# Performance work log

Measured on AMD Instinct MI355X. Metric: run time of the kernel, lower is better.

The kernel has to match this reference:

```python
import jax, jax.numpy as jnp
import numpy as np

HEADS = 16
KV_HEADS = 4
DIM_HEAD = 64
DIM = 1024
B, N = 2, 2048


def setup_inputs() -> dict:
    key = jax.random.key(0)
    k1, k2, k3 = jax.random.split(key, 3)
    x = jax.random.normal(k1, (B, N, DIM), dtype=jnp.float32)
    Wq = jax.random.normal(k2, (DIM, HEADS * DIM_HEAD), dtype=jnp.float32) / np.sqrt(DIM)
    Wkv = jax.random.normal(k3, (DIM, 2 * KV_HEADS * DIM_HEAD), dtype=jnp.float32) / np.sqrt(DIM)
    k_scale = jnp.ones((HEADS, 1, DIM_HEAD), dtype=jnp.float32)
    return {"x": x, "Wq": Wq, "Wkv": Wkv, "k_scale": k_scale}


def reference(x, Wq, Wkv, k_scale):
    b, n, _ = x.shape
    g = HEADS // KV_HEADS  # query heads per kv head
    scale = DIM_HEAD ** -0.5
    # fused qkv projections (no bias)
    q = (x @ Wq).reshape(b, n, HEADS, DIM_HEAD)
    kv = x @ Wkv
    k, v = jnp.split(kv, 2, axis=-1)
    k = k.reshape(b, n, KV_HEADS, DIM_HEAD).transpose(0, 2, 1, 3)  # b k n d
    v = v.reshape(b, n, KV_HEADS, DIM_HEAD).transpose(0, 2, 1, 3)  # b k n d
    # group query heads: b, kv_heads, g, n, d
    qg = q.transpose(0, 2, 1, 3).reshape(b, KV_HEADS, g, n, DIM_HEAD)
    # per-query-head k scale, applied to the group-broadcast k (qk-norm)
    ks = k_scale.reshape(KV_HEADS, g, 1, DIM_HEAD)
    kk = k[:, :, None, :, :] * ks  # b k g n d
    dots = jnp.einsum('bkgid,bkgjd->bkgij', qg, kk) * scale
    attn = jax.nn.softmax(dots, axis=-1)
    out = jnp.einsum('bkgij,bkjd->bkgid', attn, v)  # v broadcast over g
    out = out.reshape(b, HEADS, n, DIM_HEAD).transpose(0, 2, 1, 3).reshape(b, n, HEADS * DIM_HEAD)
    return out
```

## Files before the change

### kernel.cpp

```cpp
#include <hip/hip_runtime.h>
#include <stdint.h>
#include <math.h>

typedef __attribute__((ext_vector_type(8))) __bf16 bf16x8;
typedef __attribute__((ext_vector_type(4))) float f32x4;
typedef __attribute__((ext_vector_type(16))) float f32x16;

__device__ __forceinline__ uint32_t f32_to_bf16_rne(float f) {
  union { float f; uint32_t u; } v; v.f = f;
  return (v.u + 0x7FFFu + ((v.u >> 16) & 1u)) >> 16;
}

__device__ __forceinline__ uint32_t cvt_pk_bf16(float lo, float hi) {
  uint32_t r;
  asm("v_cvt_pk_bf16_f32 %0, %1, %2" : "=v"(r) : "v"(lo), "v"(hi));
  return r;
}

__device__ __forceinline__ void gld16(void* lds, const void* g) {
  __builtin_amdgcn_global_load_lds(
      (__attribute__((address_space(1))) void*)(g),
      (__attribute__((address_space(3))) void*)(lds), 16, 0, 0);
}

__device__ __forceinline__ f32x4 mfma16(bf16x8 a, bf16x8 b, f32x4 c) {
  return __builtin_amdgcn_mfma_f32_16x16x32_bf16(a, b, c, 0, 0, 0);
}
__device__ __forceinline__ f32x16 mfma32(bf16x8 a, bf16x8 b, f32x16 c) {
  return __builtin_amdgcn_mfma_f32_32x32x16_bf16(a, b, c, 0, 0, 0);
}

#define LOG2E 1.44269504088896340736f

__global__ __launch_bounds__(256) void k_convert_x(const float* __restrict__ x,
                                                   uint16_t* __restrict__ xb) {
  int i = blockIdx.x * 256 + threadIdx.x;
  const float4* xv = (const float4*)x;
  float4 a = xv[2 * i], b2 = xv[2 * i + 1];
  uint32_t w0 = f32_to_bf16_rne(a.x) | (f32_to_bf16_rne(a.y) << 16);
  uint32_t w1 = f32_to_bf16_rne(a.z) | (f32_to_bf16_rne(a.w) << 16);
  uint32_t w2 = f32_to_bf16_rne(b2.x) | (f32_to_bf16_rne(b2.y) << 16);
  uint32_t w3 = f32_to_bf16_rne(b2.z) | (f32_to_bf16_rne(b2.w) << 16);
  ((uint4*)xb)[i] = make_uint4(w0, w1, w2, w3);
}

__global__ __launch_bounds__(256) void k_convert_w(const float* __restrict__ wq,
                                                   const float* __restrict__ wkv,
                                                   uint16_t* __restrict__ wt) {
  __shared__ float tile[64][65];
  int c0 = blockIdx.x * 64, k0 = blockIdx.y * 64;
  int t = threadIdx.x;
  int col = t & 63, rq = t >> 6;
#pragma unroll
  for (int rr = 0; rr < 16; rr++) {
    int r = rr * 4 + rq;
    int c = c0 + col;
    float v = (c < 1024) ? wq[(uint64_t)(k0 + r) * 1024 + c]
                         : wkv[(uint64_t)(k0 + r) * 512 + (c - 1024)];
    tile[r][col] = v;
  }
  __syncthreads();
#pragma unroll
  for (int rr = 0; rr < 16; rr++) {
    int a = rr * 4 + rq;
    wt[(uint64_t)(c0 + a) * 1024 + k0 + col] = (uint16_t)f32_to_bf16_rne(tile[col][a]);
  }
}

__global__ __launch_bounds__(256, 3) void k_proj_gemm(
    const uint16_t* __restrict__ xb, const uint16_t* __restrict__ wt,
    const float* __restrict__ kscale, uint16_t* __restrict__ q_ws,
    uint16_t* __restrict__ kf_ws, uint16_t* __restrict__ vf_ws) {
  __shared__ __align__(16) uint16_t As[2][128 * 32];
  __shared__ __align__(16) uint16_t Bs[2][64 * 32];
  int t = threadIdx.x;
  int w = t >> 6, l = t & 63;
  int lq = l & 15, lg = l >> 4;
  int m0 = blockIdx.x * 128, n0 = blockIdx.y * 64;
  int wr = w >> 1, wc = w & 1;
  f32x4 acc[4][2] = {};

  auto stage = [&](int buf, int k0) {
#pragma unroll
    for (int j = 0; j < 2; j++) {
      int tt = j * 256 + t;
      int r = tt >> 2, s = tt & 3;
      int sl = s ^ ((r >> 1) & 3);
      gld16((char*)&As[buf][0] + (j * 256 + w * 64) * 16,
            xb + (uint64_t)(m0 + r) * 1024 + k0 + sl * 8);
    }
    {
      int r = t >> 2, s = t & 3;
      int sl = s ^ ((r >> 1) & 3);
      gld16((char*)&Bs[buf][0] + (w * 64) * 16,
            wt + (uint64_t)(n0 + r) * 1024 + k0 + sl * 8);
    }
  };

  stage(0, 0);
  asm volatile("s_waitcnt vmcnt(0)" ::: "memory");
  __builtin_amdgcn_s_barrier();
  int cur = 0;
  for (int k0 = 0; k0 < 1024; k0 += 32) {
    if (k0 + 32 < 1024) stage(cur ^ 1, k0 + 32);
    bf16x8 af[4], bfr[2];
#pragma unroll
    for (int m = 0; m < 4; m++) {
      int r = wr * 64 + m * 16 + lq;
      int s = lg ^ ((r >> 1) & 3);
      af[m] = *(const bf16x8*)(&As[cur][r * 32 + s * 8]);
    }
#pragma unroll
    for (int n = 0; n < 2; n++) {
      int r = wc * 32 + n * 16 + lq;
      int s = lg ^ ((r >> 1) & 3);
      bfr[n] = *(const bf16x8*)(&Bs[cur][r * 32 + s * 8]);
    }
    __builtin_amdgcn_s_setprio(1);
#pragma unroll
    for (int m = 0; m < 4; m++)
#pragma unroll
      for (int n = 0; n < 2; n++)
        acc[m][n] = mfma16(af[m], bfr[n], acc[m][n]);
    __builtin_amdgcn_s_setprio(0);
    asm volatile("s_waitcnt vmcnt(0) lgkmcnt(0)" ::: "memory");
    __builtin_amdgcn_s_barrier();
    cur ^= 1;
  }

#pragma unroll
  for (int m = 0; m < 4; m++)
#pragma unroll
    for (int n = 0; n < 2; n++)
#pragma unroll
      for (int jj = 0; jj < 4; jj++) {
        int row = m0 + wr * 64 + m * 16 + 4 * lg + jj;
        int col = n0 + wc * 32 + n * 16 + lq;
        float val = acc[m][n][jj];
        int b = row >> 11, nn = row & 2047;
        if (col < 1024) {
          val *= kscale[col] * 0.125f * LOG2E;
          q_ws[((uint64_t)((b * 16 + (col >> 6)) * 2048 + nn)) * 64 + (col & 63)] =
              (uint16_t)f32_to_bf16_rne(val);
        } else if (col < 1280) {
          int kvh = (col - 1024) >> 6;
          int d = col & 63;
          int gsu = nn >> 5, lrr = nn & 31;
          int mm = d >> 4, hh = (d >> 3) & 1, el = d & 7;
          kf_ws[(uint64_t)(b * 4 + kvh) * 131072 +
                (uint64_t)((((gsu * 4 + mm) * 64) + hh * 32 + lrr) * 8 + el)] =
              (uint16_t)f32_to_bf16_rne(val);
        } else {
          int kvh = (col - 1280) >> 6;
          int d = col & 63;
          int gsu = nn >> 5, jj2 = (nn >> 4) & 1, hh = (nn >> 3) & 1, el = nn & 7;
          int dd = d >> 5, lrr = d & 31;
          vf_ws[(uint64_t)(b * 4 + kvh) * 131072 +
                (uint64_t)((((gsu * 4 + dd * 2 + jj2) * 64) + hh * 32 + lrr) * 8 + el)] =
              (uint16_t)f32_to_bf16_rne(val);
        }
      }
}

__global__ __launch_bounds__(512, 4) void k_attn(const uint16_t* __restrict__ q_ws,
                                                 const uint16_t* __restrict__ kf_ws,
                                                 const uint16_t* __restrict__ vf_ws,
                                                 float* __restrict__ out) {
  __shared__ __align__(16) char smem[33280];

  int t = threadIdx.x, w = t >> 6, l = t & 63;
  int lr = l & 31, hi = l >> 5;
  int wq = w & 3, half = w >> 2;
  int blk = blockIdx.x;
  int c = blk & 7, j = blk >> 3;
  int b = c >> 2, kvh = c & 3;
  int h = kvh * 4 + (j >> 4), qb = j & 15;

  const uint16_t* Qb = q_ws + (uint64_t)(b * 16 + h) * 2048 * 64;
  const uint16_t* Kp =
      kf_ws + (uint64_t)(b * 4 + kvh) * 131072 + (uint64_t)half * 65536 + l * 8;
  const uint16_t* Vp =
      vf_ws + (uint64_t)(b * 4 + kvh) * 131072 + (uint64_t)half * 65536 + l * 8;
  int qrow0 = qb * 128 + wq * 32;

  bf16x8 qfrag[4];
#pragma unroll
  for (int m = 0; m < 4; m++)
    qfrag[m] = *(const bf16x8*)(Qb + (uint64_t)(qrow0 + lr) * 64 + m * 16 + hi * 8);

  f32x16 oacc[2] = {};
  float l_run = 0.f;

  bf16x8 kf[4], vf[4];
#pragma unroll
  for (int i = 0; i < 4; i++) kf[i] = *(const bf16x8*)(Kp + i * 512);
#pragma unroll
  for (int i = 0; i < 4; i++) vf[i] = *(const bf16x8*)(Vp + i * 512);

  for (int su = 0; su < 32; ++su) {
    f32x16 Tacc = {};
    __builtin_amdgcn_s_setprio(1);
#pragma unroll
    for (int m = 0; m < 4; m++) Tacc = mfma32(kf[m], qfrag[m], Tacc);
    __builtin_amdgcn_s_setprio(0);

    if (su != 31) {
#pragma unroll
      for (int i = 0; i < 4; i++)
        kf[i] = *(const bf16x8*)(Kp + (su + 1) * 2048 + i * 512);
    }

    float p[16];
#pragma unroll
    for (int e = 0; e < 16; e++) p[e] = __builtin_amdgcn_exp2f(Tacc[e]);
    float sm0 = ((p[0] + p[1]) + (p[2] + p[3])) + ((p[4] + p[5]) + (p[6] + p[7]));
    float sm1 = ((p[8] + p[9]) + (p[10] + p[11])) + ((p[12] + p[13]) + (p[14] + p[15]));
    l_run += sm0 + sm1;

    bf16x8 pa[2];
#pragma unroll
    for (int jj = 0; jj < 2; jj++) {
      int base = 8 * jj;
      uint32_t wlo0 = cvt_pk_bf16(p[base + 0], p[base + 1]);
      uint32_t wlo1 = cvt_pk_bf16(p[base + 2], p[base + 3]);
      uint32_t whi0 = cvt_pk_bf16(p[base + 4], p[base + 5]);
      uint32_t whi1 = cvt_pk_bf16(p[base + 6], p[base + 7]);
      uint32_t send0 = hi ? wlo0 : whi0;
      uint32_t send1 = hi ? wlo1 : whi1;
      uint32_t recv0 = (uint32_t)__shfl_xor((int)send0, 32);
      uint32_t recv1 = (uint32_t)__shfl_xor((int)send1, 32);
      union { uint32_t u[4]; bf16x8 v; } pu;
      pu.u[0] = hi ? recv0 : wlo0;
      pu.u[1] = hi ? recv1 : wlo1;
      pu.u[2] = hi ? whi0 : recv0;
      pu.u[3] = hi ? whi1 : recv1;
      pa[jj] = pu.v;
    }

    __builtin_amdgcn_s_setprio(1);
#pragma unroll
    for (int dd = 0; dd < 2; dd++)
#pragma unroll
      for (int jj = 0; jj < 2; jj++)
        oacc[dd] = mfma32(pa[jj], vf[dd * 2 + jj], oacc[dd]);
    __builtin_amdgcn_s_setprio(0);

    if (su != 31) {
#pragma unroll
      for (int i = 0; i < 4; i++)
        vf[i] = *(const bf16x8*)(Vp + (su + 1) * 2048 + i * 512);
    }
  }

  l_run += __shfl_xor(l_run, 32);

  float* exch = (float*)smem;
  float* exl = (float*)(smem + 32768);
  if (half == 1) {
#pragma unroll
    for (int r = 0; r < 16; r++) {
      int qr = (r & 3) + 8 * (r >> 2) + 4 * hi;
      exch[wq * 2048 + qr * 64 + lr] = oacc[0][r];
      exch[wq * 2048 + qr * 64 + 32 + lr] = oacc[1][r];
    }
    if (hi == 0) exl[wq * 32 + lr] = l_run;
  }
  __syncthreads();
  if (half == 0) {
    l_run += exl[wq * 32 + lr];
    float inv = 1.0f / l_run;
#pragma unroll
    for (int r = 0; r < 16; r++) {
      int qr = (r & 3) + 8 * (r >> 2) + 4 * hi;
      float iv = __shfl(inv, qr);
      float o0 = oacc[0][r] + exch[wq * 2048 + qr * 64 + lr];
      float o1 = oacc[1][r] + exch[wq * 2048 + qr * 64 + 32 + lr];
      float* orow = out + (uint64_t)(b * 2048 + qrow0 + qr) * 1024 + h * 64 + lr;
      orow[0] = o0 * iv;
      orow[32] = o1 * iv;
    }
  }
}

extern "C" void kernel_launch(void* const* d_in, const int* in_sizes, int n_in,
                              void* d_out, int out_size, void* d_ws, size_t ws_size,
                              hipStream_t stream) {
  const float* x = (const float*)d_in[0];
  const float* wq = (const float*)d_in[1];
  const float* wkv = (const float*)d_in[2];
  const float* kscale = (const float*)d_in[3];
  float* out = (float*)d_out;
  char* ws = (char*)d_ws;
  uint16_t* xb = (uint16_t*)(ws);
  uint16_t* wt = (uint16_t*)(ws + (8ull << 20));
  uint16_t* q_ws = (uint16_t*)(ws + (11ull << 20));
  uint16_t* kf_ws = (uint16_t*)(ws + (19ull << 20));
  uint16_t* vf_ws = (uint16_t*)(ws + (21ull << 20));

  k_convert_x<<<2048, 256, 0, stream>>>(x, xb);
  k_convert_w<<<dim3(24, 16), 256, 0, stream>>>(wq, wkv, wt);
  k_proj_gemm<<<dim3(32, 24), 256, 0, stream>>>(xb, wt, kscale, q_ws, kf_ws, vf_ws);
  k_attn<<<512, 512, 0, stream>>>(q_ws, kf_ws, vf_ws, out);
}
```

Before: 83.76 us.

## Triple-buffer projection GEMM and stage K/V through LDS ring in attention

The projection GEMM moves from a double buffer to a three-slot LDS ring with two stages in flight and partial vmcnt waits, so global loads overlap more compute. The attention kernel stops loading K/V fragments from global memory straight into registers. Instead its waves cooperatively stream K/V tiles into a four-slot LDS ring via global_load_lds, with a barrier every step, which grows shared memory to 64KB. The P-fragment lane exchange now uses v_permlane32_swap in place of two shuffles plus selects. Together these trade more LDS, which may lower occupancy, and extra per-iteration barriers for better latency hiding.

Measured after the change: 80.47 us. 3.9% less time.

```diff
diff --git a/kernel.cpp b/kernel.cpp
--- a/kernel.cpp
+++ b/kernel.cpp
@@ -71,8 +71,7 @@
     const uint16_t* __restrict__ xb, const uint16_t* __restrict__ wt,
     const float* __restrict__ kscale, uint16_t* __restrict__ q_ws,
     uint16_t* __restrict__ kf_ws, uint16_t* __restrict__ vf_ws) {
-  __shared__ __align__(16) uint16_t As[2][128 * 32];
-  __shared__ __align__(16) uint16_t Bs[2][64 * 32];
+  __shared__ __align__(16) uint16_t ring[3][6144];
   int t = threadIdx.x;
   int w = t >> 6, l = t & 63;
   int lq = l & 15, lg = l >> 4;
@@ -80,41 +79,48 @@
   int wr = w >> 1, wc = w & 1;
   f32x4 acc[4][2] = {};
 
-  auto stage = [&](int buf, int k0) {
+  auto stage = [&](int slot, int k0) {
 #pragma unroll
     for (int j = 0; j < 2; j++) {
       int tt = j * 256 + t;
       int r = tt >> 2, s = tt & 3;
       int sl = s ^ ((r >> 1) & 3);
-      gld16((char*)&As[buf][0] + (j * 256 + w * 64) * 16,
+      gld16((char*)&ring[slot][0] + (j * 256 + w * 64) * 16,
             xb + (uint64_t)(m0 + r) * 1024 + k0 + sl * 8);
     }
     {
       int r = t >> 2, s = t & 3;
       int sl = s ^ ((r >> 1) & 3);
-      gld16((char*)&Bs[buf][0] + (w * 64) * 16,
+      gld16((char*)&ring[slot][4096] + (w * 64) * 16,
             wt + (uint64_t)(n0 + r) * 1024 + k0 + sl * 8);
     }
   };
 
   stage(0, 0);
-  asm volatile("s_waitcnt vmcnt(0)" ::: "memory");
+  stage(1, 32);
+  asm volatile("s_waitcnt vmcnt(3)" ::: "memory");
   __builtin_amdgcn_s_barrier();
-  int cur = 0;
-  for (int k0 = 0; k0 < 1024; k0 += 32) {
-    if (k0 + 32 < 1024) stage(cur ^ 1, k0 + 32);
+
+  for (int it = 0; it < 32; ++it) {
+    int k0 = it * 32;
+    int kn = k0 + 64;
+    if (kn > 992) kn = 992;
+    stage((it + 2) % 3, kn);
+
+    const uint16_t* As = &ring[it % 3][0];
+    const uint16_t* Bs = &ring[it % 3][4096];
     bf16x8 af[4], bfr[2];
 #pragma unroll
     for (int m = 0; m < 4; m++) {
       int r = wr * 64 + m * 16 + lq;
       int s = lg ^ ((r >> 1) & 3);
-      af[m] = *(const bf16x8*)(&As[cur][r * 32 + s * 8]);
+      af[m] = *(const bf16x8*)(As + r * 32 + s * 8);
     }
 #pragma unroll
     for (int n = 0; n < 2; n++) {
       int r = wc * 32 + n * 16 + lq;
       int s = lg ^ ((r >> 1) & 3);
-      bfr[n] = *(const bf16x8*)(&Bs[cur][r * 32 + s * 8]);
+      bfr[n] = *(const bf16x8*)(Bs + r * 32 + s * 8);
     }
     __builtin_amdgcn_s_setprio(1);
 #pragma unroll
@@ -123,9 +129,8 @@
       for (int n = 0; n < 2; n++)
         acc[m][n] = mfma16(af[m], bfr[n], acc[m][n]);
     __builtin_amdgcn_s_setprio(0);
-    asm volatile("s_waitcnt vmcnt(0) lgkmcnt(0)" ::: "memory");
+    asm volatile("s_waitcnt vmcnt(3) lgkmcnt(0)" ::: "memory");
     __builtin_amdgcn_s_barrier();
-    cur ^= 1;
   }
 
 #pragma unroll
@@ -166,7 +171,7 @@
                                                  const uint16_t* __restrict__ kf_ws,
                                                  const uint16_t* __restrict__ vf_ws,
                                                  float* __restrict__ out) {
-  __shared__ __align__(16) char smem[33280];
+  __shared__ __align__(16) char smem[65536];
 
   int t = threadIdx.x, w = t >> 6, l = t & 63;
   int lr = l & 31, hi = l >> 5;
@@ -177,10 +182,8 @@
   int h = kvh * 4 + (j >> 4), qb = j & 15;
 
   const uint16_t* Qb = q_ws + (uint64_t)(b * 16 + h) * 2048 * 64;
-  const uint16_t* Kp =
-      kf_ws + (uint64_t)(b * 4 + kvh) * 131072 + (uint64_t)half * 65536 + l * 8;
-  const uint16_t* Vp =
-      vf_ws + (uint64_t)(b * 4 + kvh) * 131072 + (uint64_t)half * 65536 + l * 8;
+  const uint16_t* Kb = kf_ws + (uint64_t)(b * 4 + kvh) * 131072;
+  const uint16_t* Vb = vf_ws + (uint64_t)(b * 4 + kvh) * 131072;
   int qrow0 = qb * 128 + wq * 32;
 
   bf16x8 qfrag[4];
@@ -191,24 +194,38 @@
   f32x16 oacc[2] = {};
   float l_run = 0.f;
 
-  bf16x8 kf[4], vf[4];
-#pragma unroll
-  for (int i = 0; i < 4; i++) kf[i] = *(const bf16x8*)(Kp + i * 512);
-#pragma unroll
-  for (int i = 0; i < 4; i++) vf[i] = *(const bf16x8*)(Vp + i * 512);
+  const uint16_t* Sb = (wq < 2) ? Kb : Vb;
+  auto stage = [&](int slot, int sul) {
+    int gsu = half * 32 + sul;
+    char* dst = smem + slot * 16384 + half * 8192 + wq * 2048 + l * 16;
+    const uint16_t* src = Sb + (uint64_t)(gsu * 4 + (wq & 1) * 2) * 512 + l * 8;
+    gld16(dst, src);
+    gld16(dst + 1024, src + 512);
+  };
+
+  stage(0, 0);
+  stage(1, 1);
+  stage(2, 2);
+  asm volatile("s_waitcnt vmcnt(4)" ::: "memory");
+  __builtin_amdgcn_s_barrier();
 
   for (int su = 0; su < 32; ++su) {
+    int sn = su + 3;
+    if (sn > 31) sn = 31;
+    stage((su + 3) & 3, sn);
+
+    const uint16_t* base = (const uint16_t*)(smem + (su & 3) * 16384 + half * 8192);
+    bf16x8 kf[4], vf[4];
+#pragma unroll
+    for (int m = 0; m < 4; m++) kf[m] = *(const bf16x8*)(base + m * 512 + l * 8);
+#pragma unroll
+    for (int i = 0; i < 4; i++) vf[i] = *(const bf16x8*)(base + (4 + i) * 512 + l * 8);
+
     f32x16 Tacc = {};
     __builtin_amdgcn_s_setprio(1);
 #pragma unroll
     for (int m = 0; m < 4; m++) Tacc = mfma32(kf[m], qfrag[m], Tacc);
     __builtin_amdgcn_s_setprio(0);
-
-    if (su != 31) {
-#pragma unroll
-      for (int i = 0; i < 4; i++)
-        kf[i] = *(const bf16x8*)(Kp + (su + 1) * 2048 + i * 512);
-    }
 
     float p[16];
 #pragma unroll
@@ -220,20 +237,15 @@
     bf16x8 pa[2];
 #pragma unroll
     for (int jj = 0; jj < 2; jj++) {
-      int base = 8 * jj;
-      uint32_t wlo0 = cvt_pk_bf16(p[base + 0], p[base + 1]);
-      uint32_t wlo1 = cvt_pk_bf16(p[base + 2], p[base + 3]);
-      uint32_t whi0 = cvt_pk_bf16(p[base + 4], p[base + 5]);
-      uint32_t whi1 = cvt_pk_bf16(p[base + 6], p[base + 7]);
-      uint32_t send0 = hi ? wlo0 : whi0;
-      uint32_t send1 = hi ? wlo1 : whi1;
-      uint32_t recv0 = (uint32_t)__shfl_xor((int)send0, 32);
-      uint32_t recv1 = (uint32_t)__shfl_xor((int)send1, 32);
+      const float* pp = p + 8 * jj;
+      uint32_t X = cvt_pk_bf16(pp[0], pp[1]);
+      uint32_t Z = cvt_pk_bf16(pp[2], pp[3]);
+      uint32_t Y = cvt_pk_bf16(pp[4], pp[5]);
+      uint32_t W2 = cvt_pk_bf16(pp[6], pp[7]);
+      asm volatile("v_permlane32_swap_b32 %0, %1" : "+v"(X), "+v"(Y));
+      asm volatile("v_permlane32_swap_b32 %0, %1" : "+v"(Z), "+v"(W2));
       union { uint32_t u[4]; bf16x8 v; } pu;
-      pu.u[0] = hi ? recv0 : wlo0;
-      pu.u[1] = hi ? recv1 : wlo1;
-      pu.u[2] = hi ? whi0 : recv0;
-      pu.u[3] = hi ? whi1 : recv1;
+      pu.u[0] = X; pu.u[1] = Z; pu.u[2] = Y; pu.u[3] = W2;
       pa[jj] = pu.v;
     }
 
@@ -245,14 +257,14 @@
         oacc[dd] = mfma32(pa[jj], vf[dd * 2 + jj], oacc[dd]);
     __builtin_amdgcn_s_setprio(0);
 
-    if (su != 31) {
-#pragma unroll
-      for (int i = 0; i < 4; i++)
-        vf[i] = *(const bf16x8*)(Vp + (su + 1) * 2048 + i * 512);
-    }
+    asm volatile("s_waitcnt vmcnt(4) lgkmcnt(0)" ::: "memory");
+    __builtin_amdgcn_s_barrier();
   }
 
   l_run += __shfl_xor(l_run, 32);
+
+  asm volatile("s_waitcnt vmcnt(0)" ::: "memory");
+  __syncthreads();
 
   float* exch = (float*)smem;
   float* exl = (float*)(smem + 32768);
```
